# Performance work log

Hardware: AMD Instinct MI355X
Metric: run time of the kernel (lower is better)

## Reference

```python
import jax, jax.numpy as jnp
import numpy as np

B, N, C = 8, 1024, 768
H = 12
D = C // H            # 64
HID = int(C * 4.0)    # 3072
SCALE = D ** -0.5
EPS_LN = 1e-5
EPS_BN = 1e-5


def _layernorm(x, g, b):
    mu = jnp.mean(x, axis=-1, keepdims=True)
    var = jnp.mean(jnp.square(x - mu), axis=-1, keepdims=True)
    return (x - mu) * jax.lax.rsqrt(var + EPS_LN) * g + b


def setup_inputs() -> dict:
    key = jax.random.key(0)
    ks = jax.random.split(key, 12)
    s = lambda fan: 1.0 / np.sqrt(fan)
    inp = {
        "inputs": jax.random.normal(ks[0], (B, N, C), jnp.float32),
        "ln1_g": jnp.ones((C,), jnp.float32),
        "ln1_b": jnp.zeros((C,), jnp.float32),
        # nn.Linear(dim, 3*dim, bias=False)
        "qkv_w": jax.random.uniform(ks[1], (3 * C, C), jnp.float32, -s(C), s(C)),
        # nn.Conv2d(H, H, 1, 1) head-mixing matrix
        "conv_w": jax.random.uniform(ks[2], (H, H), jnp.float32, -s(H), s(H)),
        "conv_b": jax.random.uniform(ks[3], (H,), jnp.float32, -s(H), s(H)),
        # BatchNorm2d(H) in eval mode: affine params + running stats
        "bn_g": jnp.ones((H,), jnp.float32),
        "bn_b": jnp.zeros((H,), jnp.float32),
        "bn_rm": jnp.zeros((H,), jnp.float32),
        "bn_rv": jnp.ones((H,), jnp.float32),
        "proj_w": jax.random.uniform(ks[4], (C, C), jnp.float32, -s(C), s(C)),
        "proj_b": jax.random.uniform(ks[5], (C,), jnp.float32, -s(C), s(C)),
        "ln2_g": jnp.ones((C,), jnp.float32),
        "ln2_b": jnp.zeros((C,), jnp.float32),
        "fc1_w": jax.random.uniform(ks[6], (HID, C), jnp.float32, -s(C), s(C)),
        "fc1_b": jax.random.uniform(ks[7], (HID,), jnp.float32, -s(C), s(C)),
        "fc2_w": jax.random.uniform(ks[8], (C, HID), jnp.float32, -s(HID), s(HID)),
        "fc2_b": jax.random.uniform(ks[9], (C,), jnp.float32, -s(HID), s(HID)),
    }
    return inp


def reference(inputs, ln1_g, ln1_b, qkv_w, conv_w, conv_b, bn_g, bn_b, bn_rm, bn_rv,
              proj_w, proj_b, ln2_g, ln2_b, fc1_w, fc1_b, fc2_w, fc2_b):
    # adjust_ratio = 1.0, dropouts are identity (inference), BN uses running stats (eval)
    x_ln = _layernorm(inputs, ln1_g, ln1_b)
    qkv = (x_ln @ qkv_w.T).reshape(B, N, 3, H, D).transpose(2, 0, 3, 1, 4)
    q, k, v = qkv[0], qkv[1], qkv[2]
    attn = jax.nn.softmax(jnp.einsum('bhnd,bhmd->bhnm', q, k) * SCALE, axis=-1)
    # 1x1 conv across heads then BatchNorm2d (eval) * reatten_scale(=1.0)
    attn = jnp.einsum('oh,bhnm->bonm', conv_w, attn) + conv_b[None, :, None, None]
    bn_scale = bn_g * jax.lax.rsqrt(bn_rv + EPS_BN)
    attn = (attn - bn_rm[None, :, None, None]) * bn_scale[None, :, None, None] \
        + bn_b[None, :, None, None]
    attn_next = attn
    out = jnp.einsum('bhnm,bhmd->bhnd', attn, v).transpose(0, 2, 1, 3).reshape(B, N, C)
    out = out @ proj_w.T + proj_b
    x = inputs + out
    h = _layernorm(x, ln2_g, ln2_b)
    h = jax.nn.gelu(h @ fc1_w.T + fc1_b, approximate=False)
    x = x + (h @ fc2_w.T + fc2_b)
    return (x, attn_next)
```

## Files before the change

kernel.cpp:

```cpp
#include <hip/hip_runtime.h>
#include <cmath>

#define B_   8
#define N_   1024
#define C_   768
#define H_   12
#define D_   64
#define HID_ 3072
#define M_   8192

using frag  = __attribute__((ext_vector_type(8))) short;
using f32x4 = __attribute__((ext_vector_type(4))) float;
using s4v   = __attribute__((ext_vector_type(4))) short;

__device__ __forceinline__ short f2bf(float x) {
    union { float f; unsigned u; } v; v.f = x;
    unsigned r = (v.u + 0x7FFFu + ((v.u >> 16) & 1u)) >> 16;
    return (short)r;
}
__device__ __forceinline__ float b2f(short s) {
    union { float f; unsigned u; } v; v.u = ((unsigned)(unsigned short)s) << 16;
    return v.f;
}
__device__ __forceinline__ float bfr(float x) { return b2f(f2bf(x)); }
__device__ __forceinline__ float gelu_exact(float x) {
    return 0.5f * x * (1.0f + erff(x * 0.70710678118654752f));
}
__device__ __forceinline__ void gload16(const void* g, void* l) {
    __builtin_amdgcn_global_load_lds(
        (const __attribute__((address_space(1))) void*)g,
        (__attribute__((address_space(3))) void*)l, 16, 0, 0);
}

__device__ __forceinline__ int2 swz_xy() {
    const int gx = gridDim.x;
    const int nwg = gx * gridDim.y;
    const int orig = blockIdx.y * gx + blockIdx.x;
    const int q = nwg >> 3, r = nwg & 7;
    const int xcd = orig & 7;
    const int base = (xcd < r) ? xcd * (q + 1) : r * (q + 1) + (xcd - r) * q;
    const int wgid = base + (orig >> 3);
    int2 v; v.x = wgid % gx; v.y = wgid / gx;
    return v;
}

#define NW0 (3 * C_ * C_)
#define NW1 (C_ * C_)
#define NW2 (HID_ * C_)
#define NW3 (C_ * HID_)
__global__ __launch_bounds__(256)
void cvt_weights(const float* __restrict__ s0, const float* __restrict__ s1,
                 const float* __restrict__ s2, const float* __restrict__ s3,
                 short* __restrict__ dst)
{
    long i = ((long)blockIdx.x * 256 + threadIdx.x) * 4;
    const float* s; long off;
    if      (i < NW0)             { s = s0; off = i; }
    else if (i < NW0 + NW1)       { s = s1; off = i - NW0; }
    else if (i < NW0 + NW1 + NW2) { s = s2; off = i - NW0 - NW1; }
    else                          { s = s3; off = i - NW0 - NW1 - NW2; }
    float4 u = *(const float4*)(s + off);
    s4v o; o[0] = f2bf(u.x); o[1] = f2bf(u.y); o[2] = f2bf(u.z); o[3] = f2bf(u.w);
    *(s4v*)(dst + i) = o;
}

__global__ __launch_bounds__(256)
void ln_bf16(const float* __restrict__ x, const float* __restrict__ g,
             const float* __restrict__ b, short* __restrict__ y)
{
    __shared__ float red[256];
    const long row = blockIdx.x;
    const float* xr = x + row * C_;
    short* yr = y + row * C_;
    const int t = threadIdx.x;
    float v0 = xr[t], v1 = xr[t + 256], v2 = xr[t + 512];
    red[t] = v0 + v1 + v2;
    __syncthreads();
    for (int o = 128; o > 0; o >>= 1) { if (t < o) red[t] += red[t + o]; __syncthreads(); }
    const float mu = red[0] * (1.0f / 768.0f);
    __syncthreads();
    const float d0 = v0 - mu, d1 = v1 - mu, d2 = v2 - mu;
    red[t] = d0 * d0 + d1 * d1 + d2 * d2;
    __syncthreads();
    for (int o = 128; o > 0; o >>= 1) { if (t < o) red[t] += red[t + o]; __syncthreads(); }
    const float rstd = rsqrtf(red[0] * (1.0f / 768.0f) + 1e-5f);
    yr[t]       = f2bf(d0 * rstd * g[t]       + b[t]);
    yr[t + 256] = f2bf(d1 * rstd * g[t + 256] + b[t + 256]);
    yr[t + 512] = f2bf(d2 * rstd * g[t + 512] + b[t + 512]);
}

template<int BM, int BN, int WGM, int WGN, bool OUTF32, bool ACT_GELU, bool STATS>
__global__ __launch_bounds__(256)
void gemm_mfma(const short* __restrict__ Ap, int lda, long sAb, long sAh,
               const short* __restrict__ Bp, int ldb, long sBb, long sBh,
               const float* __restrict__ bias,
               const float* __restrict__ res, int ldres,
               void* __restrict__ Cp, int ldc, long sCb, long sCh,
               float2* __restrict__ st,
               int K, float alpha)
{
    constexpr int FM = BM / (WGM * 16), FN = BN / (WGN * 16);
    __shared__ short As[BM * 64];
    __shared__ short Bs[BN * 64];
    const int tid = threadIdx.x;
    const int wid = tid >> 6, lane = tid & 63;
    const int z = blockIdx.z, zb = z / H_, zh = z - zb * H_;
    const int2 bxy = swz_xy();
    const int bx = bxy.x, by = bxy.y;
    const long m0 = (long)by * BM;
    const int  n0 = bx * BN;
    const short* Ab = Ap + zb * sAb + zh * sAh + m0 * lda;
    const short* Bb = Bp + zb * sBb + zh * sBh + (long)n0 * ldb;
    f32x4 acc[FM][FN] = {};
    const int wr = wid / WGN, wc = wid - wr * WGN;
    const int srow = lane >> 3;
    const int schunk = (lane & 7) ^ srow;

    for (int k0 = 0; k0 < K; k0 += 64) {
        for (int g = wid; g < BM / 8; g += 4)
            gload16(Ab + (long)(g * 8 + srow) * lda + k0 + schunk * 8, &As[g * 512]);
        for (int g = wid; g < BN / 8; g += 4)
            gload16(Bb + (long)(g * 8 + srow) * ldb + k0 + schunk * 8, &Bs[g * 512]);
        __syncthreads();
        #pragma unroll
        for (int kk = 0; kk < 2; ++kk) {
            frag a[FM], b[FN];
            #pragma unroll
            for (int fm = 0; fm < FM; ++fm) {
                const int r = wr * FM * 16 + fm * 16 + (lane & 15);
                const int ph = (kk * 4 + (lane >> 4)) ^ (r & 7);
                a[fm] = *(const frag*)&As[r * 64 + ph * 8];
            }
            #pragma unroll
            for (int fn = 0; fn < FN; ++fn) {
                const int r = wc * FN * 16 + fn * 16 + (lane & 15);
                const int ph = (kk * 4 + (lane >> 4)) ^ (r & 7);
                b[fn] = *(const frag*)&Bs[r * 64 + ph * 8];
            }
            #pragma unroll
            for (int fm = 0; fm < FM; ++fm)
                #pragma unroll
                for (int fn = 0; fn < FN; ++fn)
                    acc[fm][fn] = __builtin_amdgcn_mfma_f32_16x16x32_bf16(a[fm], b[fn], acc[fm][fn], 0, 0, 0);
        }
        __syncthreads();
    }

    float* Cf = (float*)Cp; short* Cs = (short*)Cp;
    const long cbase = zb * sCb + zh * sCh;
    #pragma unroll
    for (int fm = 0; fm < FM; ++fm) {
        #pragma unroll
        for (int fn = 0; fn < FN; ++fn) {
            const long rg = m0 + wr * FM * 16 + fm * 16 + ((lane >> 4) * 4);
            const int  cg = n0 + wc * FN * 16 + fn * 16 + (lane & 15);
            const float bv = bias ? bias[cg] : 0.0f;
            #pragma unroll
            for (int q = 0; q < 4; ++q) {
                const long row = rg + q;
                float v = acc[fm][fn][q] * alpha + bv;
                if (res) v += res[row * (long)ldres + cg];
                if constexpr (ACT_GELU) v = gelu_exact(v);
                if constexpr (OUTF32) Cf[cbase + row * ldc + cg] = v;
                else                  Cs[cbase + row * ldc + cg] = f2bf(v);
            }
        }
    }

    if constexpr (STATS) {
        float* sred = (float*)As;
        float tmax[FM][4];
        #pragma unroll
        for (int fm = 0; fm < FM; ++fm)
            #pragma unroll
            for (int q = 0; q < 4; ++q) {
                float v = bfr(acc[fm][0][q] * alpha);
                #pragma unroll
                for (int fn = 1; fn < FN; ++fn) v = fmaxf(v, bfr(acc[fm][fn][q] * alpha));
                v = fmaxf(v, __shfl_xor(v, 1));
                v = fmaxf(v, __shfl_xor(v, 2));
                v = fmaxf(v, __shfl_xor(v, 4));
                v = fmaxf(v, __shfl_xor(v, 8));
                const int r = wr * FM * 16 + fm * 16 + (lane >> 4) * 4 + q;
                if ((lane & 15) == 0) sred[wc * BM + r] = v;
            }
        __syncthreads();
        #pragma unroll
        for (int fm = 0; fm < FM; ++fm)
            #pragma unroll
            for (int q = 0; q < 4; ++q) {
                const int r = wr * FM * 16 + fm * 16 + (lane >> 4) * 4 + q;
                tmax[fm][q] = fmaxf(sred[r], sred[BM + r]);
            }
        __syncthreads();
        #pragma unroll
        for (int fm = 0; fm < FM; ++fm)
            #pragma unroll
            for (int q = 0; q < 4; ++q) {
                float e = 0.0f;
                #pragma unroll
                for (int fn = 0; fn < FN; ++fn)
                    e += __expf(bfr(acc[fm][fn][q] * alpha) - tmax[fm][q]);
                e += __shfl_xor(e, 1);
                e += __shfl_xor(e, 2);
                e += __shfl_xor(e, 4);
                e += __shfl_xor(e, 8);
                const int r = wr * FM * 16 + fm * 16 + (lane >> 4) * 4 + q;
                if ((lane & 15) == 0) sred[wc * BM + r] = e;
            }
        __syncthreads();
        if (wc == 0) {
            #pragma unroll
            for (int fm = 0; fm < FM; ++fm)
                #pragma unroll
                for (int q = 0; q < 4; ++q) {
                    const int r = wr * FM * 16 + fm * 16 + (lane >> 4) * 4 + q;
                    if ((lane & 15) == 0) {
                        float2 o; o.x = tmax[fm][q]; o.y = sred[r] + sred[BM + r];
                        st[((long)z * N_ + m0 + r) * 8 + bx] = o;
                    }
                }
        }
    }
}

__global__ __launch_bounds__(256)
void smb2(short* __restrict__ S, const float2* __restrict__ st,
          float* __restrict__ attn,
          const float* __restrict__ cw, const float* __restrict__ cb,
          const float* __restrict__ bg, const float* __restrict__ bb,
          const float* __restrict__ brm, const float* __restrict__ brv)
{
    __shared__ float coef[H_][H_], baseA[H_], scA[H_], smx[H_], sinv[H_];
    const int t = threadIdx.x;
    const int bn = blockIdx.x;
    const int b = bn >> 10, n = bn & 1023;
    if (t < H_) {
        const float s = bg[t] * rsqrtf(brv[t] + 1e-5f);
        scA[t] = s;
        baseA[t] = (cb[t] - brm[t]) * s + bb[t];
    }
    __syncthreads();
    if (t < H_ * H_) coef[t / H_][t % H_] = cw[t] * scA[t / H_];
    if (t < H_) {
        const float2* sp = st + ((long)(b * H_ + t) * N_ + n) * 8;
        float2 sv[8];
        #pragma unroll
        for (int i = 0; i < 8; ++i) sv[i] = sp[i];
        float gm = sv[0].x;
        #pragma unroll
        for (int i = 1; i < 8; ++i) gm = fmaxf(gm, sv[i].x);
        float gs = 0.0f;
        #pragma unroll
        for (int i = 0; i < 8; ++i) gs += sv[i].y * __expf(sv[i].x - gm);
        smx[t] = gm;
        sinv[t] = 1.0f / gs;
    }
    __syncthreads();

    const long pstr = (long)N_ * N_;
    short*       sb = S    + (long)b * H_ * pstr + (long)n * N_ + t * 4;
    float*       ab = attn + (long)b * H_ * pstr + (long)n * N_ + t * 4;
    float4 p[H_];
    #pragma unroll
    for (int h = 0; h < H_; ++h) {
        const s4v sv = *(const s4v*)(sb + (long)h * pstr);
        const float gm = smx[h], gi = sinv[h];
        float4 e;
        e.x = __expf(b2f(sv[0]) - gm) * gi;
        e.y = __expf(b2f(sv[1]) - gm) * gi;
        e.z = __expf(b2f(sv[2]) - gm) * gi;
        e.w = __expf(b2f(sv[3]) - gm) * gi;
        p[h] = e;
    }
    #pragma unroll
    for (int o = 0; o < H_; ++o) {
        const float bse = baseA[o];
        float4 a; a.x = bse; a.y = bse; a.z = bse; a.w = bse;
        #pragma unroll
        for (int h = 0; h < H_; ++h) {
            const float w = coef[o][h];
            a.x += w * p[h].x; a.y += w * p[h].y;
            a.z += w * p[h].z; a.w += w * p[h].w;
        }
        *(float4*)(ab + (long)o * pstr) = a;
        s4v pb; pb[0] = f2bf(a.x); pb[1] = f2bf(a.y); pb[2] = f2bf(a.z); pb[3] = f2bf(a.w);
        *(s4v*)(sb + (long)o * pstr) = pb;
    }
}

__global__ __launch_bounds__(256)
void vtrans(const short* __restrict__ qkv, short* __restrict__ vT)
{
    __shared__ short tile[64][72];
    const int bh = blockIdx.x;
    const int n0 = blockIdx.y * 64;
    const int b = bh / H_, h = bh - b * H_;
    const short* src = qkv + (long)b * N_ * (3 * C_) + 2 * C_ + h * D_;
    const int t = threadIdx.x;
    {
        const int r = t >> 2, c = (t & 3) * 16;
        const short* sp = src + (long)(n0 + r) * (3 * C_) + c;
        #pragma unroll
        for (int j = 0; j < 16; j++) tile[r][c + j] = sp[j];
    }
    __syncthreads();
    {
        const int d = t >> 2, c = (t & 3) * 16;
        short* dp = vT + (long)bh * (D_ * N_) + (long)d * N_ + n0 + c;
        #pragma unroll
        for (int j = 0; j < 16; j++) dp[j] = tile[c + j][d];
    }
}

extern "C" void kernel_launch(void* const* d_in, const int* in_sizes, int n_in,
                              void* d_out, int out_size, void* d_ws, size_t ws_size,
                              hipStream_t stream)
{
    const float* inp    = (const float*)d_in[0];
    const float* ln1_g  = (const float*)d_in[1];
    const float* ln1_b  = (const float*)d_in[2];
    const float* qkv_w  = (const float*)d_in[3];
    const float* conv_w = (const float*)d_in[4];
    const float* conv_b = (const float*)d_in[5];
    const float* bn_g   = (const float*)d_in[6];
    const float* bn_b   = (const float*)d_in[7];
    const float* bn_rm  = (const float*)d_in[8];
    const float* bn_rv  = (const float*)d_in[9];
    const float* proj_w = (const float*)d_in[10];
    const float* proj_b = (const float*)d_in[11];
    const float* ln2_g  = (const float*)d_in[12];
    const float* ln2_b  = (const float*)d_in[13];
    const float* fc1_w  = (const float*)d_in[14];
    const float* fc1_b  = (const float*)d_in[15];
    const float* fc2_w  = (const float*)d_in[16];
    const float* fc2_b  = (const float*)d_in[17];

    float* outx = (float*)d_out;
    float* attn = outx + (long)M_ * C_;

    char* w = (char*)d_ws;
    short* wqkv  = (short*)w;  w += (long)NW0 * 2;
    short* wproj = (short*)w;  w += (long)NW1 * 2;
    short* wfc1  = (short*)w;  w += (long)NW2 * 2;
    short* wfc2  = (short*)w;  w += (long)NW3 * 2;
    short* xln   = (short*)w;  w += (long)M_ * C_ * 2;
    short* qkvb  = (short*)w;
    short* hbuf  = qkvb;       w += (long)M_ * HID_ * 2;
    short* vT    = (short*)w;  w += (long)B_ * H_ * D_ * N_ * 2;
    short* Obf   = (short*)w;  w += (long)M_ * C_ * 2;
    float* xres  = (float*)w;  w += (long)M_ * C_ * 4;
    float2* st   = (float2*)w; w += (long)B_ * H_ * N_ * 8 * 8;
    short* Sbf   = (short*)w;  w += (long)B_ * H_ * N_ * N_ * 2;

    cvt_weights<<<(NW0 + NW1 + NW2 + NW3) / 1024, 256, 0, stream>>>(
        qkv_w, proj_w, fc1_w, fc2_w, wqkv);

    ln_bf16<<<M_, 256, 0, stream>>>(inp, ln1_g, ln1_b, xln);

    gemm_mfma<128, 128, 2, 2, false, false, false><<<dim3(18, 64, 1), 256, 0, stream>>>(
        xln, C_, 0, 0, wqkv, C_, 0, 0, nullptr, nullptr, 0,
        qkvb, 3 * C_, 0, 0, nullptr, C_, 1.0f);

    vtrans<<<dim3(B_ * H_, 16), 256, 0, stream>>>(qkvb, vT);

    gemm_mfma<128, 128, 2, 2, false, false, true><<<dim3(8, 8, 96), 256, 0, stream>>>(
        qkvb,      3 * C_, (long)N_ * 3 * C_, D_,
        qkvb + C_, 3 * C_, (long)N_ * 3 * C_, D_,
        nullptr, nullptr, 0,
        Sbf, N_, (long)H_ * N_ * N_, (long)N_ * N_, st, D_, 0.125f);

    smb2<<<M_, 256, 0, stream>>>(Sbf, st, attn, conv_w, conv_b, bn_g, bn_b, bn_rm, bn_rv);

    gemm_mfma<128, 64, 4, 1, false, false, false><<<dim3(1, 8, 96), 256, 0, stream>>>(
        Sbf, N_, (long)H_ * N_ * N_, (long)N_ * N_,
        vT, N_, (long)H_ * D_ * N_, (long)D_ * N_,
        nullptr, nullptr, 0,
        Obf, C_, (long)N_ * C_, D_, nullptr, N_, 1.0f);

    gemm_mfma<128, 128, 2, 2, true, false, false><<<dim3(6, 64, 1), 256, 0, stream>>>(
        Obf, C_, 0, 0, wproj, C_, 0, 0, proj_b, inp, C_,
        xres, C_, 0, 0, nullptr, C_, 1.0f);

    ln_bf16<<<M_, 256, 0, stream>>>(xres, ln2_g, ln2_b, xln);

    gemm_mfma<128, 128, 2, 2, false, true, false><<<dim3(24, 64, 1), 256, 0, stream>>>(
        xln, C_, 0, 0, wfc1, C_, 0, 0, fc1_b, nullptr, 0,
        hbuf, HID_, 0, 0, nullptr, C_, 1.0f);

    gemm_mfma<128, 128, 2, 2, true, false, false><<<dim3(6, 64, 1), 256, 0, stream>>>(
        hbuf, HID_, 0, 0, wfc2, HID_, 0, 0, fc2_b, xres, C_,
        outx, C_, 0, 0, nullptr, HID_, 1.0f);
}
```

Before: 611.6 us.

## Recompute QK scores in fused softmax-headmix kernel and drop bf16 score buffer

The QK GEMM now only produces per-row softmax statistics and no longer writes the full bf16 score matrix. A new kernel recomputes QK^T per 16x64 tile across all heads, applies softmax, head mixing and BN, and streams the fp32 attention output with nontemporal stores. The PV GEMM then reads that fp32 attention directly and converts it to bf16 on the fly. The proj and fc2 GEMMs switch to 128x64 tiles, with a nontemporal store for the final output. This removes the large intermediate score round-trip through memory at the cost of recomputing QK, and stats are now taken from unrounded fp32 values.

Result: faster. 545.0 us (-10.9%).

```diff
diff --git a/kernel.cpp b/kernel.cpp
--- a/kernel.cpp
+++ b/kernel.cpp
@@ -18,11 +18,6 @@
     unsigned r = (v.u + 0x7FFFu + ((v.u >> 16) & 1u)) >> 16;
     return (short)r;
 }
-__device__ __forceinline__ float b2f(short s) {
-    union { float f; unsigned u; } v; v.u = ((unsigned)(unsigned short)s) << 16;
-    return v.f;
-}
-__device__ __forceinline__ float bfr(float x) { return b2f(f2bf(x)); }
 __device__ __forceinline__ float gelu_exact(float x) {
     return 0.5f * x * (1.0f + erff(x * 0.70710678118654752f));
 }
@@ -89,9 +84,10 @@
     yr[t + 512] = f2bf(d2 * rstd * g[t + 512] + b[t + 512]);
 }
 
-template<int BM, int BN, int WGM, int WGN, bool OUTF32, bool ACT_GELU, bool STATS>
+template<int BM, int BN, int WGM, int WGN, bool AF32, bool OUTF32,
+         bool ACT_GELU, bool STATS, bool CW, bool NTC, int GMODE>
 __global__ __launch_bounds__(256)
-void gemm_mfma(const short* __restrict__ Ap, int lda, long sAb, long sAh,
+void gemm_mfma(const void* __restrict__ Ap, int lda, long sAb, long sAh,
                const short* __restrict__ Bp, int ldb, long sBb, long sBh,
                const float* __restrict__ bias,
                const float* __restrict__ res, int ldres,
@@ -104,21 +100,44 @@
     __shared__ short Bs[BN * 64];
     const int tid = threadIdx.x;
     const int wid = tid >> 6, lane = tid & 63;
-    const int z = blockIdx.z, zb = z / H_, zh = z - zb * H_;
-    const int2 bxy = swz_xy();
-    const int bx = bxy.x, by = bxy.y;
+    int bx, by, z;
+    if constexpr (GMODE == 1) {
+        const int nwg = gridDim.x;
+        const int qc = nwg >> 3;
+        const int wg = (blockIdx.x & 7) * qc + (blockIdx.x >> 3);
+        bx = 0; by = wg & 7; z = wg >> 3;
+    } else {
+        int2 v = swz_xy(); bx = v.x; by = v.y; z = blockIdx.z;
+    }
+    const int zb = z / H_, zh = z - zb * H_;
     const long m0 = (long)by * BM;
     const int  n0 = bx * BN;
-    const short* Ab = Ap + zb * sAb + zh * sAh + m0 * lda;
     const short* Bb = Bp + zb * sBb + zh * sBh + (long)n0 * ldb;
+    const short* Abh = nullptr; const float* Afh = nullptr;
+    if constexpr (AF32) Afh = (const float*)Ap + zb * sAb + zh * sAh + m0 * lda;
+    else                Abh = (const short*)Ap + zb * sAb + zh * sAh + m0 * lda;
     f32x4 acc[FM][FN] = {};
     const int wr = wid / WGN, wc = wid - wr * WGN;
     const int srow = lane >> 3;
     const int schunk = (lane & 7) ^ srow;
 
     for (int k0 = 0; k0 < K; k0 += 64) {
-        for (int g = wid; g < BM / 8; g += 4)
-            gload16(Ab + (long)(g * 8 + srow) * lda + k0 + schunk * 8, &As[g * 512]);
+        if constexpr (!AF32) {
+            for (int g = wid; g < BM / 8; g += 4)
+                gload16(Abh + (long)(g * 8 + srow) * lda + k0 + schunk * 8, &As[g * 512]);
+        } else {
+            const int r = tid >> 1, h2 = tid & 1;
+            const float* sp = Afh + (long)r * lda + k0 + h2 * 32;
+            #pragma unroll
+            for (int j = 0; j < 4; ++j) {
+                float4 u0 = *(const float4*)(sp + j * 8);
+                float4 u1 = *(const float4*)(sp + j * 8 + 4);
+                frag w;
+                w[0] = f2bf(u0.x); w[1] = f2bf(u0.y); w[2] = f2bf(u0.z); w[3] = f2bf(u0.w);
+                w[4] = f2bf(u1.x); w[5] = f2bf(u1.y); w[6] = f2bf(u1.z); w[7] = f2bf(u1.w);
+                *(frag*)&As[r * 64 + ((h2 * 4 + j) ^ (r & 7)) * 8] = w;
+            }
+        }
         for (int g = wid; g < BN / 8; g += 4)
             gload16(Bb + (long)(g * 8 + srow) * ldb + k0 + schunk * 8, &Bs[g * 512]);
         __syncthreads();
@@ -146,23 +165,29 @@
         __syncthreads();
     }
 
-    float* Cf = (float*)Cp; short* Cs = (short*)Cp;
-    const long cbase = zb * sCb + zh * sCh;
-    #pragma unroll
-    for (int fm = 0; fm < FM; ++fm) {
-        #pragma unroll
-        for (int fn = 0; fn < FN; ++fn) {
-            const long rg = m0 + wr * FM * 16 + fm * 16 + ((lane >> 4) * 4);
-            const int  cg = n0 + wc * FN * 16 + fn * 16 + (lane & 15);
-            const float bv = bias ? bias[cg] : 0.0f;
-            #pragma unroll
-            for (int q = 0; q < 4; ++q) {
-                const long row = rg + q;
-                float v = acc[fm][fn][q] * alpha + bv;
-                if (res) v += res[row * (long)ldres + cg];
-                if constexpr (ACT_GELU) v = gelu_exact(v);
-                if constexpr (OUTF32) Cf[cbase + row * ldc + cg] = v;
-                else                  Cs[cbase + row * ldc + cg] = f2bf(v);
+    if constexpr (CW) {
+        float* Cf = (float*)Cp; short* Cs = (short*)Cp;
+        const long cbase = zb * sCb + zh * sCh;
+        #pragma unroll
+        for (int fm = 0; fm < FM; ++fm) {
+            #pragma unroll
+            for (int fn = 0; fn < FN; ++fn) {
+                const long rg = m0 + wr * FM * 16 + fm * 16 + ((lane >> 4) * 4);
+                const int  cg = n0 + wc * FN * 16 + fn * 16 + (lane & 15);
+                const float bv = bias ? bias[cg] : 0.0f;
+                #pragma unroll
+                for (int q = 0; q < 4; ++q) {
+                    const long row = rg + q;
+                    float v = acc[fm][fn][q] * alpha + bv;
+                    if (res) v += res[row * (long)ldres + cg];
+                    if constexpr (ACT_GELU) v = gelu_exact(v);
+                    if constexpr (OUTF32) {
+                        if constexpr (NTC) __builtin_nontemporal_store(v, &Cf[cbase + row * ldc + cg]);
+                        else               Cf[cbase + row * ldc + cg] = v;
+                    } else {
+                        Cs[cbase + row * ldc + cg] = f2bf(v);
+                    }
+                }
             }
         }
     }
@@ -174,9 +199,10 @@
         for (int fm = 0; fm < FM; ++fm)
             #pragma unroll
             for (int q = 0; q < 4; ++q) {
-                float v = bfr(acc[fm][0][q] * alpha);
+                float v = acc[fm][0][q];
                 #pragma unroll
-                for (int fn = 1; fn < FN; ++fn) v = fmaxf(v, bfr(acc[fm][fn][q] * alpha));
+                for (int fn = 1; fn < FN; ++fn) v = fmaxf(v, acc[fm][fn][q]);
+                v *= alpha;
                 v = fmaxf(v, __shfl_xor(v, 1));
                 v = fmaxf(v, __shfl_xor(v, 2));
                 v = fmaxf(v, __shfl_xor(v, 4));
@@ -200,7 +226,7 @@
                 float e = 0.0f;
                 #pragma unroll
                 for (int fn = 0; fn < FN; ++fn)
-                    e += __expf(bfr(acc[fm][fn][q] * alpha) - tmax[fm][q]);
+                    e += __expf(acc[fm][fn][q] * alpha - tmax[fm][q]);
                 e += __shfl_xor(e, 1);
                 e += __shfl_xor(e, 2);
                 e += __shfl_xor(e, 4);
@@ -225,25 +251,32 @@
 }
 
 __global__ __launch_bounds__(256)
-void smb2(short* __restrict__ S, const float2* __restrict__ st,
+void qksm(const short* __restrict__ qkvb, const float2* __restrict__ st,
           float* __restrict__ attn,
           const float* __restrict__ cw, const float* __restrict__ cb,
           const float* __restrict__ bg, const float* __restrict__ bb,
           const float* __restrict__ brm, const float* __restrict__ brv)
 {
-    __shared__ float coef[H_][H_], baseA[H_], scA[H_], smx[H_], sinv[H_];
-    const int t = threadIdx.x;
-    const int bn = blockIdx.x;
-    const int b = bn >> 10, n = bn & 1023;
-    if (t < H_) {
-        const float s = bg[t] * rsqrtf(brv[t] + 1e-5f);
-        scA[t] = s;
-        baseA[t] = (cb[t] - brm[t]) * s + bb[t];
-    }
-    __syncthreads();
-    if (t < H_ * H_) coef[t / H_][t % H_] = cw[t] * scA[t / H_];
-    if (t < H_) {
-        const float2* sp = st + ((long)(b * H_ + t) * N_ + n) * 8;
+    __shared__ short qs[H_ * 16 * 64];
+    __shared__ short ks[2][64 * 64];
+    __shared__ float smx[H_][16], sinv[H_][16];
+    __shared__ float coef[H_][H_], baseA[H_], scA[H_];
+    const int tid = threadIdx.x, wid = tid >> 6, lane = tid & 63;
+
+    const int wg = (blockIdx.x & 7) * 1024 + (blockIdx.x >> 3);
+    const int b = wg >> 10, nblk = (wg >> 4) & 63, mblk = wg & 15;
+    const int n0 = nblk * 16, m0 = mblk * 64;
+
+    if (tid < H_) {
+        const float s = bg[tid] * rsqrtf(brv[tid] + 1e-5f);
+        scA[tid] = s;
+        baseA[tid] = (cb[tid] - brm[tid]) * s + bb[tid];
+    }
+    __syncthreads();
+    if (tid < H_ * H_) coef[tid / H_][tid % H_] = cw[tid] * scA[tid / H_];
+    if (tid < 192) {
+        const int h = tid >> 4, r = tid & 15;
+        const float2* sp = st + ((long)(b * H_ + h) * N_ + n0 + r) * 8;
         float2 sv[8];
         #pragma unroll
         for (int i = 0; i < 8; ++i) sv[i] = sp[i];
@@ -253,39 +286,62 @@
         float gs = 0.0f;
         #pragma unroll
         for (int i = 0; i < 8; ++i) gs += sv[i].y * __expf(sv[i].x - gm);
-        smx[t] = gm;
-        sinv[t] = 1.0f / gs;
-    }
-    __syncthreads();
-
-    const long pstr = (long)N_ * N_;
-    short*       sb = S    + (long)b * H_ * pstr + (long)n * N_ + t * 4;
-    float*       ab = attn + (long)b * H_ * pstr + (long)n * N_ + t * 4;
-    float4 p[H_];
-    #pragma unroll
+        smx[h][r] = gm;
+        sinv[h][r] = 1.0f / gs;
+    }
+    __syncthreads();
+
+    const int srow = lane >> 3, schunk = (lane & 7) ^ srow;
+    const short* qbase = qkvb + (long)(b * N_ + n0) * (3 * C_);
+    for (int g = wid; g < 24; g += 4) {
+        const int fr = g * 8 + srow;
+        gload16(qbase + (long)(fr & 15) * (3 * C_) + (fr >> 4) * 64 + schunk * 8,
+                &qs[g * 512]);
+    }
+    const short* kbase = qkvb + C_ + (long)(b * N_ + m0) * (3 * C_);
+    for (int g = wid; g < 8; g += 4) {
+        const int fr = g * 8 + srow;
+        gload16(kbase + (long)fr * (3 * C_) + schunk * 8, &ks[0][g * 512]);
+    }
+
+    float macc[H_][4] = {};
+    const int rowb = (lane >> 4) * 4;
+    const int colw = wid * 16 + (lane & 15);
+
     for (int h = 0; h < H_; ++h) {
-        const s4v sv = *(const s4v*)(sb + (long)h * pstr);
-        const float gm = smx[h], gi = sinv[h];
-        float4 e;
-        e.x = __expf(b2f(sv[0]) - gm) * gi;
-        e.y = __expf(b2f(sv[1]) - gm) * gi;
-        e.z = __expf(b2f(sv[2]) - gm) * gi;
-        e.w = __expf(b2f(sv[3]) - gm) * gi;
-        p[h] = e;
-    }
+        asm volatile("s_waitcnt vmcnt(0)" ::: "memory");
+        __builtin_amdgcn_sched_barrier(0);
+        __builtin_amdgcn_s_barrier();
+        if (h < H_ - 1) {
+            for (int g = wid; g < 8; g += 4) {
+                const int fr = g * 8 + srow;
+                gload16(kbase + (long)fr * (3 * C_) + (h + 1) * 64 + schunk * 8,
+                        &ks[(h + 1) & 1][g * 512]);
+            }
+        }
+        f32x4 acc = {};
+        const int afr = h * 16 + (lane & 15);
+        const int bfr = colw;
+        #pragma unroll
+        for (int kk = 0; kk < 2; ++kk) {
+            const frag a  = *(const frag*)&qs[afr * 64 + (((kk * 4 + (lane >> 4)) ^ (afr & 7))) * 8];
+            const frag bv = *(const frag*)&ks[h & 1][bfr * 64 + (((kk * 4 + (lane >> 4)) ^ (bfr & 7))) * 8];
+            acc = __builtin_amdgcn_mfma_f32_16x16x32_bf16(a, bv, acc, 0, 0, 0);
+        }
+        #pragma unroll
+        for (int q = 0; q < 4; ++q) {
+            const float e = __expf(acc[q] * 0.125f - smx[h][rowb + q]) * sinv[h][rowb + q];
+            #pragma unroll
+            for (int o = 0; o < H_; ++o) macc[o][q] += coef[o][h] * e;
+        }
+    }
+
     #pragma unroll
     for (int o = 0; o < H_; ++o) {
-        const float bse = baseA[o];
-        float4 a; a.x = bse; a.y = bse; a.z = bse; a.w = bse;
-        #pragma unroll
-        for (int h = 0; h < H_; ++h) {
-            const float w = coef[o][h];
-            a.x += w * p[h].x; a.y += w * p[h].y;
-            a.z += w * p[h].z; a.w += w * p[h].w;
-        }
-        *(float4*)(ab + (long)o * pstr) = a;
-        s4v pb; pb[0] = f2bf(a.x); pb[1] = f2bf(a.y); pb[2] = f2bf(a.z); pb[3] = f2bf(a.w);
-        *(s4v*)(sb + (long)o * pstr) = pb;
+        float* ap = attn + ((long)(b * H_ + o) << 20) + ((long)(n0 + rowb) << 10) + m0 + colw;
+        #pragma unroll
+        for (int q = 0; q < 4; ++q)
+            __builtin_nontemporal_store(macc[o][q] + baseA[o], ap + ((long)q << 10));
     }
 }
 
@@ -351,44 +407,50 @@
     short* Obf   = (short*)w;  w += (long)M_ * C_ * 2;
     float* xres  = (float*)w;  w += (long)M_ * C_ * 4;
     float2* st   = (float2*)w; w += (long)B_ * H_ * N_ * 8 * 8;
-    short* Sbf   = (short*)w;  w += (long)B_ * H_ * N_ * N_ * 2;
 
     cvt_weights<<<(NW0 + NW1 + NW2 + NW3) / 1024, 256, 0, stream>>>(
         qkv_w, proj_w, fc1_w, fc2_w, wqkv);
 
     ln_bf16<<<M_, 256, 0, stream>>>(inp, ln1_g, ln1_b, xln);
 
-    gemm_mfma<128, 128, 2, 2, false, false, false><<<dim3(18, 64, 1), 256, 0, stream>>>(
+    gemm_mfma<128, 128, 2, 2, false, false, false, false, true, false, 0>
+        <<<dim3(18, 64, 1), 256, 0, stream>>>(
         xln, C_, 0, 0, wqkv, C_, 0, 0, nullptr, nullptr, 0,
         qkvb, 3 * C_, 0, 0, nullptr, C_, 1.0f);
 
     vtrans<<<dim3(B_ * H_, 16), 256, 0, stream>>>(qkvb, vT);
 
-    gemm_mfma<128, 128, 2, 2, false, false, true><<<dim3(8, 8, 96), 256, 0, stream>>>(
+    gemm_mfma<128, 128, 2, 2, false, false, false, true, false, false, 0>
+        <<<dim3(8, 8, 96), 256, 0, stream>>>(
         qkvb,      3 * C_, (long)N_ * 3 * C_, D_,
         qkvb + C_, 3 * C_, (long)N_ * 3 * C_, D_,
         nullptr, nullptr, 0,
-        Sbf, N_, (long)H_ * N_ * N_, (long)N_ * N_, st, D_, 0.125f);
-
-    smb2<<<M_, 256, 0, stream>>>(Sbf, st, attn, conv_w, conv_b, bn_g, bn_b, bn_rm, bn_rv);
-
-    gemm_mfma<128, 64, 4, 1, false, false, false><<<dim3(1, 8, 96), 256, 0, stream>>>(
-        Sbf, N_, (long)H_ * N_ * N_, (long)N_ * N_,
+        nullptr, N_, 0, 0, st, D_, 0.125f);
+
+    qksm<<<8192, 256, 0, stream>>>(qkvb, st, attn,
+                                   conv_w, conv_b, bn_g, bn_b, bn_rm, bn_rv);
+
+    gemm_mfma<128, 64, 4, 1, true, false, false, false, true, false, 1>
+        <<<dim3(768, 1, 1), 256, 0, stream>>>(
+        attn, N_, (long)H_ * N_ * N_, (long)N_ * N_,
         vT, N_, (long)H_ * D_ * N_, (long)D_ * N_,
         nullptr, nullptr, 0,
         Obf, C_, (long)N_ * C_, D_, nullptr, N_, 1.0f);
 
-    gemm_mfma<128, 128, 2, 2, true, false, false><<<dim3(6, 64, 1), 256, 0, stream>>>(
+    gemm_mfma<128, 64, 4, 1, false, true, false, false, true, false, 0>
+        <<<dim3(12, 64, 1), 256, 0, stream>>>(
         Obf, C_, 0, 0, wproj, C_, 0, 0, proj_b, inp, C_,
         xres, C_, 0, 0, nullptr, C_, 1.0f);
 
     ln_bf16<<<M_, 256, 0, stream>>>(xres, ln2_g, ln2_b, xln);
 
-    gemm_mfma<128, 128, 2, 2, false, true, false><<<dim3(24, 64, 1), 256, 0, stream>>>(
+    gemm_mfma<128, 128, 2, 2, false, false, true, false, true, false, 0>
+        <<<dim3(24, 64, 1), 256, 0, stream>>>(
         xln, C_, 0, 0, wfc1, C_, 0, 0, fc1_b, nullptr, 0,
         hbuf, HID_, 0, 0, nullptr, C_, 1.0f);
 
-    gemm_mfma<128, 128, 2, 2, true, false, false><<<dim3(6, 64, 1), 256, 0, stream>>>(
+    gemm_mfma<128, 64, 4, 1, false, true, false, false, true, true, 0>
+        <<<dim3(12, 64, 1), 256, 0, stream>>>(
         hbuf, HID_, 0, 0, wfc2, HID_, 0, 0, fc2_b, xres, C_,
         outx, C_, 0, 0, nullptr, HID_, 1.0f);
 }
```
